# Kernel optimization log

Hardware: AMD Instinct MI355X
Metric: run time of the kernel (lower is better)

The kernel has to match this reference:

```python
import jax, jax.numpy as jnp
import numpy as np

N = 256          # num agents
HID = 128        # hidden_dim
ACT = 5          # action_dim
NH = 4           # num_heads
D = HID + 16     # concat_hidden_dim = 144
E = D * NH       # mha embed dim = 576
HD = D           # per-head dim = E // NH = 144
OBS_RX, OBS_RY = 4, 2   # obs_r from fov_size=(9,5)
GRID = 40


def setup_inputs() -> dict:
    key = jax.random.key(0)
    ks = jax.random.split(key, 24)
    g = lambda k, shape, s: (jax.random.normal(k, shape, dtype=jnp.float32) * s)
    inp = {
        "hidden_state_n": g(ks[0], (N, HID), 1.0),
        "action_n": g(ks[1], (N, HID), 1.0),
        "state_n": jax.random.randint(ks[2], (N, 2), 0, GRID, dtype=jnp.int32),
        # obs encoder
        "W_enc": g(ks[3], (HID, 16), HID ** -0.5), "b_enc": jnp.zeros((16,), jnp.float32),
        # MHABlock outer projections
        "Wq": g(ks[4], (D, E), D ** -0.5), "bq": jnp.zeros((E,), jnp.float32),
        "Wk": g(ks[5], (D, E), D ** -0.5), "bk": jnp.zeros((E,), jnp.float32),
        "Wv": g(ks[6], (D, E), D ** -0.5), "bv": jnp.zeros((E,), jnp.float32),
        # nn.MultiheadAttention internal in/out projections
        "Wiq": g(ks[7], (E, E), E ** -0.5), "biq": jnp.zeros((E,), jnp.float32),
        "Wik": g(ks[8], (E, E), E ** -0.5), "bik": jnp.zeros((E,), jnp.float32),
        "Wiv": g(ks[9], (E, E), E ** -0.5), "biv": jnp.zeros((E,), jnp.float32),
        "Wo_proj": g(ks[10], (E, E), E ** -0.5), "bo_proj": jnp.zeros((E,), jnp.float32),
        "W_O": g(ks[11], (E, D), E ** -0.5),  # no bias
        # dueling decoders
        "W_val": g(ks[12], (D, 1), D ** -0.5), "b_val": jnp.zeros((1,), jnp.float32),
        "W_adv": g(ks[13], (D, ACT), D ** -0.5), "b_adv": jnp.zeros((ACT,), jnp.float32),
    }
    return inp


def reference(hidden_state_n, action_n, W_enc, b_enc, Wq, bq, Wk, bk, Wv, bv,
              Wiq, biq, Wik, bik, Wiv, biv, Wo_proj, bo_proj, W_O,
              W_val, b_val, W_adv, b_adv, state_n):
    n = hidden_state_n.shape[0]
    # observed_agents[i] = {j > i : |x_i-x_j|<=rx and |y_i-y_j|<=ry}
    pos = state_n.astype(jnp.int32)
    dx = jnp.abs(pos[:, None, 0] - pos[None, :, 0])
    dy = jnp.abs(pos[:, None, 1] - pos[None, :, 1])
    upper = jnp.arange(n)[None, :] > jnp.arange(n)[:, None]
    mask = (dx <= OBS_RX) & (dy <= OBS_RY) & upper            # [N,N], mask[i,j]: j observed by i

    # per-neighbor feature c_j = concat(obs_encoder(h_j), a_j)  -> [N, D]
    obs = hidden_state_n @ W_enc + b_enc                       # [N,16]
    C = jnp.concatenate([obs, action_n], axis=-1)              # [N,D]

    # MHABlock: outer Q/K/V projections then nn.MultiheadAttention
    q = (C @ Wq + bq) @ Wiq + biq                              # [N,E]
    k = (C @ Wk + bk) @ Wik + bik
    v = (C @ Wv + bv) @ Wiv + biv
    q2 = q.reshape(n, NH, HD)
    k2 = k.reshape(n, NH, HD)
    v2 = v.reshape(n, NH, HD)

    scale = 1.0 / np.sqrt(HD).astype(np.float32)
    S = jnp.einsum("jhd,khd->hjk", q2, k2) * scale             # [H,N,N] shared across agents

    pair = (mask[:, None, :, None] & mask[:, None, None, :])   # [N,1,Nq,Nk]
    logits = jnp.where(pair, S[None, :, :, :], -1e9)           # [N,H,N,N]
    m = jnp.max(logits, axis=-1, keepdims=True)
    p = jnp.exp(logits - m) * pair.astype(logits.dtype)
    attn = p / jnp.maximum(p.sum(axis=-1, keepdims=True), 1e-9)

    ctx = jnp.einsum("ihjk,khd->ijhd", attn, v2).reshape(n, n, E)  # [N,Nq,E]
    out = (ctx @ Wo_proj + bo_proj) @ W_O                          # [N,Nq,D]

    # sum over the (masked) neighbor/query axis -> per-agent h_i
    h = jnp.sum(out * mask[:, :, None].astype(out.dtype), axis=1)  # [N,D]

    V = h @ W_val + b_val                                          # [N,1]
    A = h @ W_adv + b_adv                                          # [N,ACT]
    Q = V + A - jnp.mean(A, axis=-1, keepdims=True)                # dueling Q
    return Q
```

## Files before the change

### kernel.cpp

```cpp
#include <hip/hip_runtime.h>
#include <hip/hip_bf16.h>

#define NAG 256
#define HID 128
#define ACT 5
#define NH 4
#define DD 144
#define EE 576
#define HDIM 144
#define CMAX 20

template<int KDIM>
__global__ __launch_bounds__(256) void k_gemmK(
    const float* __restrict__ A0, const float* __restrict__ A1, const float* __restrict__ A2,
    const float* __restrict__ W0, const float* __restrict__ W1, const float* __restrict__ W2,
    const float* __restrict__ bb0, const float* __restrict__ bb1, const float* __restrict__ bb2,
    const float* __restrict__ bscale,
    float* __restrict__ o0, float* __restrict__ o1, float* __restrict__ o2,
    int N, int NX)
{
    constexpr int Kc = KDIM / 4;
    constexpr int G  = (Kc % 16 == 0) ? 16 : 12;
    constexpr int NG = Kc / G;
    constexpr int LDA = KDIM + 4;
    __shared__ union { float As[8 * LDA]; float red[2048]; } sm;

    const int perz = NX * 32;
    const int b = blockIdx.x;
    const int z = b / perz, rem = b % perz;
    const int bx = rem >> 5, mb = rem & 31;
    const float* A   = (z == 0) ? A0  : (z == 1) ? A1  : A2;
    const float* W   = (z == 0) ? W0  : (z == 1) ? W1  : W2;
    const float* bia = (z == 0) ? bb0 : (z == 1) ? bb1 : bb2;
    float*       out = (z == 0) ? o0  : (z == 1) ? o1  : o2;
    const int tid = threadIdx.x;

    for (int idx = tid; idx < 8 * (KDIM / 4); idx += 256) {
        int r = idx / (KDIM / 4), c = idx % (KDIM / 4);
        *((float4*)&sm.As[r * LDA + c * 4]) =
            *(const float4*)(A + (size_t)(mb * 8 + r) * KDIM + c * 4);
    }
    __syncthreads();

    const int wave = tid >> 6, lane = tid & 63;
    const int colg = bx * 64 + lane;
    const bool cv = colg < N;
    const int colc = cv ? colg : (N - 1);
    const float* Wp = W + (size_t)(wave * Kc) * N + colc;
    float acc[8] = {};
    float wv[G], wn[G];
    #pragma unroll
    for (int j = 0; j < G; ++j) wv[j] = Wp[(size_t)j * N];
    for (int g = 0; g < NG; ++g) {
        if (g + 1 < NG) {
            const float* Wn = Wp + (size_t)(g + 1) * G * N;
            #pragma unroll
            for (int j = 0; j < G; ++j) wn[j] = Wn[(size_t)j * N];
        }
        const int kb = wave * Kc + g * G;
        #pragma unroll
        for (int j4 = 0; j4 < G / 4; ++j4) {
            #pragma unroll
            for (int r = 0; r < 8; ++r) {
                float4 a4 = *(const float4*)&sm.As[r * LDA + kb + j4 * 4];
                acc[r] += a4.x * wv[j4 * 4 + 0] + a4.y * wv[j4 * 4 + 1]
                        + a4.z * wv[j4 * 4 + 2] + a4.w * wv[j4 * 4 + 3];
            }
        }
        #pragma unroll
        for (int j = 0; j < G; ++j) wv[j] = wn[j];
    }
    __syncthreads();
    #pragma unroll
    for (int r = 0; r < 8; ++r) sm.red[wave * 512 + r * 64 + lane] = acc[r];
    __syncthreads();
    #pragma unroll
    for (int q = 0; q < 2; ++q) {
        int idx = tid + q * 256;
        int r = idx >> 6, cl = idx & 63;
        int col = bx * 64 + cl;
        if (col < N) {
            float s = sm.red[idx] + sm.red[512 + idx]
                    + sm.red[1024 + idx] + sm.red[1536 + idx];
            int row = mb * 8 + r;
            float bs = bscale ? bscale[row] : 1.f;
            float bb = bia ? bia[col] : 0.f;
            out[(size_t)row * N + col] = s + bs * bb;
        }
    }
}

__global__ __launch_bounds__(256) void k_gemm1(
    const float* __restrict__ hidden, const float* __restrict__ action,
    const float* __restrict__ W_enc, const float* __restrict__ b_enc,
    const float* __restrict__ Wq, const float* __restrict__ Wk, const float* __restrict__ Wv,
    const float* __restrict__ bq, const float* __restrict__ bk, const float* __restrict__ bv,
    float* __restrict__ tq, float* __restrict__ tk, float* __restrict__ tv)
{
    __shared__ float Ct[8][148];
    __shared__ union { struct { float Hs[8][132]; float We[2048]; } e;
                       float red[2048]; } u;
    const int b = blockIdx.x;
    const int z = b / 288, rem = b % 288;
    const int bx = rem >> 5, mb = rem & 31;
    const float* W  = (z == 0) ? Wq : (z == 1) ? Wk : Wv;
    const float* bi = (z == 0) ? bq : (z == 1) ? bk : bv;
    float*      out = (z == 0) ? tq : (z == 1) ? tk : tv;
    const int tid = threadIdx.x;

    {
        int r = tid >> 5, kq = tid & 31;
        *((float4*)&u.e.Hs[r][kq * 4]) =
            *(const float4*)(hidden + (mb * 8 + r) * HID + kq * 4);
        *((float4*)&Ct[r][16 + kq * 4]) =
            *(const float4*)(action + (mb * 8 + r) * HID + kq * 4);
        *((float4*)&u.e.We[tid * 4])       = *(const float4*)(W_enc + tid * 4);
        *((float4*)&u.e.We[1024 + tid * 4]) = *(const float4*)(W_enc + 1024 + tid * 4);
    }
    __syncthreads();
    if (tid < 128) {
        int r = tid >> 4, o = tid & 15;
        float acc = 0.f;
        #pragma unroll 8
        for (int d = 0; d < HID; ++d) acc += u.e.Hs[r][d] * u.e.We[d * 16 + o];
        Ct[r][o] = acc + b_enc[o];
    }
    __syncthreads();

    constexpr int Kc = 36, G = 12, NG = 3;
    const int wave = tid >> 6, lane = tid & 63;
    const int colg = bx * 64 + lane;
    const float* Wp = W + (size_t)(wave * Kc) * EE + colg;
    float acc[8] = {};
    float wv[G], wn[G];
    #pragma unroll
    for (int j = 0; j < G; ++j) wv[j] = Wp[(size_t)j * EE];
    for (int g = 0; g < NG; ++g) {
        if (g + 1 < NG) {
            const float* Wn = Wp + (size_t)(g + 1) * G * EE;
            #pragma unroll
            for (int j = 0; j < G; ++j) wn[j] = Wn[(size_t)j * EE];
        }
        const int kb = wave * Kc + g * G;
        #pragma unroll
        for (int j4 = 0; j4 < G / 4; ++j4) {
            #pragma unroll
            for (int r = 0; r < 8; ++r) {
                float4 a4 = *(const float4*)&Ct[r][kb + j4 * 4];
                acc[r] += a4.x * wv[j4 * 4 + 0] + a4.y * wv[j4 * 4 + 1]
                        + a4.z * wv[j4 * 4 + 2] + a4.w * wv[j4 * 4 + 3];
            }
        }
        #pragma unroll
        for (int j = 0; j < G; ++j) wv[j] = wn[j];
    }
    __syncthreads();
    #pragma unroll
    for (int r = 0; r < 8; ++r) u.red[wave * 512 + r * 64 + lane] = acc[r];
    __syncthreads();
    #pragma unroll
    for (int q = 0; q < 2; ++q) {
        int idx = tid + q * 256;
        int r = idx >> 6, cl = idx & 63;
        int col = bx * 64 + cl;
        float s = u.red[idx] + u.red[512 + idx]
                + u.red[1024 + idx] + u.red[1536 + idx];
        out[(size_t)(mb * 8 + r) * EE + col] = s + bi[col];
    }
}

__global__ __launch_bounds__(256) void k_attn(
    const int* __restrict__ state, const float* __restrict__ q,
    const float* __restrict__ kmat, const float* __restrict__ v,
    float* __restrict__ ctxsum, float* __restrict__ cnt)
{
    __shared__ int lst[NAG];
    __shared__ int cnt_s;
    __shared__ float w4[NH][NAG];
    __shared__ float qh[CMAX][HDIM + 1];
    __shared__ float kh[CMAX][HDIM + 1];
    __shared__ float Sl[CMAX][CMAX + 1];
    const int i = blockIdx.x, tid = threadIdx.x;
    if (tid == 0) cnt_s = 0;
    __syncthreads();
    {
        int xi = state[2 * i], yi = state[2 * i + 1];
        int xj = state[2 * tid], yj = state[2 * tid + 1];
        int dx = xi - xj; if (dx < 0) dx = -dx;
        int dy = yi - yj; if (dy < 0) dy = -dy;
        if (tid > i && dx <= 4 && dy <= 2) {
            int p = atomicAdd(&cnt_s, 1);
            lst[p] = tid;
        }
    }
    __syncthreads();
    const int c = cnt_s;
    if (tid == 0) cnt[i] = (float)c;
    if (c == 0) {
        for (int e = tid; e < EE; e += 256) ctxsum[i * EE + e] = 0.f;
        return;
    }
    if (c <= CMAX) {
        for (int h = 0; h < NH; ++h) {
            for (int idx = tid; idx < c * HDIM; idx += 256) {
                int jj = idx / HDIM, d = idx % HDIM;
                qh[jj][d] = q[lst[jj] * EE + h * HDIM + d];
                kh[jj][d] = kmat[lst[jj] * EE + h * HDIM + d];
            }
            __syncthreads();
            for (int pp = tid; pp < c * c; pp += 256) {
                int jj = pp / c, kk = pp % c;
                float acc = 0.f;
                for (int d = 0; d < HDIM; ++d) acc += qh[jj][d] * kh[kk][d];
                Sl[jj][kk] = acc * (1.0f / 12.0f);
            }
            __syncthreads();
            if (tid < c) {
                float m = -1e30f;
                for (int kk = 0; kk < c; ++kk) m = fmaxf(m, Sl[tid][kk]);
                float zz = 0.f;
                for (int kk = 0; kk < c; ++kk) zz += __expf(Sl[tid][kk] - m);
                float inv = 1.f / fmaxf(zz, 1e-9f);
                for (int kk = 0; kk < c; ++kk)
                    Sl[tid][kk] = __expf(Sl[tid][kk] - m) * inv;
            }
            __syncthreads();
            if (tid < c) {
                float s = 0.f;
                for (int jj = 0; jj < c; ++jj) s += Sl[jj][tid];
                w4[h][tid] = s;
            }
            __syncthreads();
        }
    } else {
        for (int idx = tid; idx < NH * c; idx += 256) w4[idx / c][idx % c] = 0.f;
        __syncthreads();
        for (int pnh = tid; pnh < NH * c; pnh += 256) {
            int h = pnh / c, jj = pnh % c;
            const float* qrow = q + lst[jj] * EE + h * HDIM;
            float m = -1e30f;
            for (int kk = 0; kk < c; ++kk) {
                const float* krow = kmat + lst[kk] * EE + h * HDIM;
                float a = 0.f;
                for (int d = 0; d < HDIM; ++d) a += qrow[d] * krow[d];
                m = fmaxf(m, a * (1.0f / 12.0f));
            }
            float zz = 0.f;
            for (int kk = 0; kk < c; ++kk) {
                const float* krow = kmat + lst[kk] * EE + h * HDIM;
                float a = 0.f;
                for (int d = 0; d < HDIM; ++d) a += qrow[d] * krow[d];
                zz += __expf(a * (1.0f / 12.0f) - m);
            }
            float inv = 1.f / fmaxf(zz, 1e-9f);
            for (int kk = 0; kk < c; ++kk) {
                const float* krow = kmat + lst[kk] * EE + h * HDIM;
                float a = 0.f;
                for (int d = 0; d < HDIM; ++d) a += qrow[d] * krow[d];
                atomicAdd(&w4[h][kk], __expf(a * (1.0f / 12.0f) - m) * inv);
            }
        }
        __syncthreads();
    }
    for (int e = tid; e < EE; e += 256) {
        int h = e / HDIM;
        float acc = 0.f;
        for (int t = 0; t < c; ++t) acc += w4[h][t] * v[lst[t] * EE + e];
        ctxsum[i * EE + e] = acc;
    }
}

__global__ __launch_bounds__(64) void k_head(
    const float* __restrict__ hb,
    const float* __restrict__ W_val, const float* __restrict__ b_val,
    const float* __restrict__ W_adv, const float* __restrict__ b_adv,
    float* __restrict__ out)
{
    const int i = blockIdx.x, t = threadIdx.x;
    const float* hr = hb + i * DD;
    float h0 = hr[t], h1 = hr[t + 64];
    float h2 = (t < 16) ? hr[t + 128] : 0.f;
    float red[6];
    for (int o = 0; o < 6; ++o) {
        float p;
        if (o < 5) {
            p = h0 * W_adv[t * ACT + o] + h1 * W_adv[(t + 64) * ACT + o];
            if (t < 16) p += h2 * W_adv[(t + 128) * ACT + o];
        } else {
            p = h0 * W_val[t] + h1 * W_val[t + 64];
            if (t < 16) p += h2 * W_val[t + 128];
        }
        for (int off = 32; off; off >>= 1) p += __shfl_xor(p, off);
        red[o] = p;
    }
    if (t == 0) {
        float a[ACT], mean = 0.f;
        for (int o = 0; o < ACT; ++o) { a[o] = red[o] + b_adv[o]; mean += a[o]; }
        mean *= (1.0f / ACT);
        float V = red[5] + b_val[0];
        for (int o = 0; o < ACT; ++o) out[i * ACT + o] = V + a[o] - mean;
    }
}

extern "C" void kernel_launch(void* const* d_in, const int* in_sizes, int n_in,
                              void* d_out, int out_size, void* d_ws, size_t ws_size,
                              hipStream_t stream)
{
    const float* hidden = (const float*)d_in[0];
    const float* action = (const float*)d_in[1];
    const int*   state  = (const int*)d_in[2];

    float* ws = (float*)d_ws;
    float* tq   = ws;
    float* tk   = tq   + NAG * EE;
    float* tv   = tk   + NAG * EE;
    float* q    = tv   + NAG * EE;
    float* kb   = q    + NAG * EE;
    float* v    = kb   + NAG * EE;
    float* ctx  = v    + NAG * EE;
    float* cnt  = ctx  + NAG * EE;
    float* hbuf = cnt  + NAG;
    float* tout = tq;

    k_gemm1<<<864, 256, 0, stream>>>(hidden, action,
        (const float*)d_in[3], (const float*)d_in[4],
        (const float*)d_in[5], (const float*)d_in[7], (const float*)d_in[9],
        (const float*)d_in[6], (const float*)d_in[8], (const float*)d_in[10],
        tq, tk, tv);

    k_gemmK<576><<<864, 256, 0, stream>>>(tq, tk, tv,
        (const float*)d_in[11], (const float*)d_in[13], (const float*)d_in[15],
        (const float*)d_in[12], (const float*)d_in[14], (const float*)d_in[16],
        nullptr, q, kb, v, EE, 9);

    k_attn<<<NAG, 256, 0, stream>>>(state, q, kb, v, ctx, cnt);

    k_gemmK<576><<<288, 256, 0, stream>>>(ctx, ctx, ctx,
        (const float*)d_in[17], (const float*)d_in[17], (const float*)d_in[17],
        (const float*)d_in[18], (const float*)d_in[18], (const float*)d_in[18],
        cnt, tout, tout, tout, EE, 9);

    k_gemmK<576><<<96, 256, 0, stream>>>(tout, tout, tout,
        (const float*)d_in[19], (const float*)d_in[19], (const float*)d_in[19],
        nullptr, nullptr, nullptr,
        nullptr, hbuf, hbuf, hbuf, DD, 3);

    k_head<<<NAG, 64, 0, stream>>>(hbuf,
        (const float*)d_in[20], (const float*)d_in[21],
        (const float*)d_in[22], (const float*)d_in[23], (float*)d_out);
}
```

Baseline: 192.1 us.

## Prefetch later-stage weights into L2 via extra blocks and enlarge register weight groups

Extra blocks are appended to the first GEMM and the attention kernel. They read the weights used by the next stage (Wiq/Wik/Wiv, then Wo_proj/W_O) so those matrices sit in cache when the following kernels run, with a dummy conditional store to keep the loads alive. The GEMM inner loops now load all 36 weight rows per wave into registers at once instead of double-buffering groups of 12 or 16. The context accumulation loop is split across two accumulators to expose more memory-level parallelism. The extra blocks add launch work and memory traffic, and the larger register arrays may lower occupancy.

```diff
diff --git a/kernel.cpp b/kernel.cpp
--- a/kernel.cpp
+++ b/kernel.cpp
@@ -20,7 +20,7 @@
     int N, int NX)
 {
     constexpr int Kc = KDIM / 4;
-    constexpr int G  = (Kc % 16 == 0) ? 16 : 12;
+    constexpr int G  = 36;
     constexpr int NG = Kc / G;
     constexpr int LDA = KDIM + 4;
     __shared__ union { float As[8 * LDA]; float red[2048]; } sm;
@@ -95,18 +95,34 @@
     const float* __restrict__ W_enc, const float* __restrict__ b_enc,
     const float* __restrict__ Wq, const float* __restrict__ Wk, const float* __restrict__ Wv,
     const float* __restrict__ bq, const float* __restrict__ bk, const float* __restrict__ bv,
-    float* __restrict__ tq, float* __restrict__ tk, float* __restrict__ tv)
-{
+    const float* __restrict__ Wiq, const float* __restrict__ Wik, const float* __restrict__ Wiv,
+    float* __restrict__ tq, float* __restrict__ tk, float* __restrict__ tv,
+    float* __restrict__ sink)
+{
+    const int b = blockIdx.x;
+    const int tid = threadIdx.x;
+    if (b >= 864) {
+        const int wb = b - 864;
+        float s = 0.f;
+        for (int m = 0; m < 3; ++m) {
+            const float* Wm = (m == 0) ? Wiq : (m == 1) ? Wik : Wiv;
+            const float4* W4 = (const float4*)Wm;
+            for (int idx = wb * 324 + tid; idx < (wb + 1) * 324 && idx < 82944; idx += 256) {
+                float4 v4 = W4[idx];
+                s += v4.x + v4.y + v4.z + v4.w;
+            }
+        }
+        if (s == 123456789.0f) sink[0] = s;
+        return;
+    }
     __shared__ float Ct[8][148];
     __shared__ union { struct { float Hs[8][132]; float We[2048]; } e;
                        float red[2048]; } u;
-    const int b = blockIdx.x;
     const int z = b / 288, rem = b % 288;
     const int bx = rem >> 5, mb = rem & 31;
     const float* W  = (z == 0) ? Wq : (z == 1) ? Wk : Wv;
     const float* bi = (z == 0) ? bq : (z == 1) ? bk : bv;
     float*      out = (z == 0) ? tq : (z == 1) ? tk : tv;
-    const int tid = threadIdx.x;
 
     {
         int r = tid >> 5, kq = tid & 31;
@@ -114,7 +130,7 @@
             *(const float4*)(hidden + (mb * 8 + r) * HID + kq * 4);
         *((float4*)&Ct[r][16 + kq * 4]) =
             *(const float4*)(action + (mb * 8 + r) * HID + kq * 4);
-        *((float4*)&u.e.We[tid * 4])       = *(const float4*)(W_enc + tid * 4);
+        *((float4*)&u.e.We[tid * 4])        = *(const float4*)(W_enc + tid * 4);
         *((float4*)&u.e.We[1024 + tid * 4]) = *(const float4*)(W_enc + 1024 + tid * 4);
     }
     __syncthreads();
@@ -127,32 +143,23 @@
     }
     __syncthreads();
 
-    constexpr int Kc = 36, G = 12, NG = 3;
+    constexpr int Kc = 36, G = 36;
     const int wave = tid >> 6, lane = tid & 63;
     const int colg = bx * 64 + lane;
     const float* Wp = W + (size_t)(wave * Kc) * EE + colg;
     float acc[8] = {};
-    float wv[G], wn[G];
+    float wv[G];
     #pragma unroll
     for (int j = 0; j < G; ++j) wv[j] = Wp[(size_t)j * EE];
-    for (int g = 0; g < NG; ++g) {
-        if (g + 1 < NG) {
-            const float* Wn = Wp + (size_t)(g + 1) * G * EE;
-            #pragma unroll
-            for (int j = 0; j < G; ++j) wn[j] = Wn[(size_t)j * EE];
-        }
-        const int kb = wave * Kc + g * G;
+    const int kb = wave * Kc;
+    #pragma unroll
+    for (int j4 = 0; j4 < G / 4; ++j4) {
         #pragma unroll
-        for (int j4 = 0; j4 < G / 4; ++j4) {
-            #pragma unroll
-            for (int r = 0; r < 8; ++r) {
-                float4 a4 = *(const float4*)&Ct[r][kb + j4 * 4];
-                acc[r] += a4.x * wv[j4 * 4 + 0] + a4.y * wv[j4 * 4 + 1]
-                        + a4.z * wv[j4 * 4 + 2] + a4.w * wv[j4 * 4 + 3];
-            }
-        }
-        #pragma unroll
-        for (int j = 0; j < G; ++j) wv[j] = wn[j];
+        for (int r = 0; r < 8; ++r) {
+            float4 a4 = *(const float4*)&Ct[r][kb + j4 * 4];
+            acc[r] += a4.x * wv[j4 * 4 + 0] + a4.y * wv[j4 * 4 + 1]
+                    + a4.z * wv[j4 * 4 + 2] + a4.w * wv[j4 * 4 + 3];
+        }
     }
     __syncthreads();
     #pragma unroll
@@ -172,15 +179,34 @@
 __global__ __launch_bounds__(256) void k_attn(
     const int* __restrict__ state, const float* __restrict__ q,
     const float* __restrict__ kmat, const float* __restrict__ v,
-    float* __restrict__ ctxsum, float* __restrict__ cnt)
-{
+    const float* __restrict__ Wo, const float* __restrict__ W_O,
+    float* __restrict__ ctxsum, float* __restrict__ cnt,
+    float* __restrict__ sink)
+{
+    const int blk = blockIdx.x, tid = threadIdx.x;
+    if (blk >= NAG) {
+        const int wb = blk - NAG;
+        float s = 0.f;
+        const float4* W4 = (const float4*)Wo;
+        for (int idx = wb * 324 + tid; idx < (wb + 1) * 324 && idx < 82944; idx += 256) {
+            float4 v4 = W4[idx];
+            s += v4.x + v4.y + v4.z + v4.w;
+        }
+        const float4* O4 = (const float4*)W_O;
+        for (int idx = wb * 81 + tid; idx < (wb + 1) * 81 && idx < 20736; idx += 256) {
+            float4 v4 = O4[idx];
+            s += v4.x + v4.y + v4.z + v4.w;
+        }
+        if (s == 123456789.0f) sink[1] = s;
+        return;
+    }
     __shared__ int lst[NAG];
     __shared__ int cnt_s;
     __shared__ float w4[NH][NAG];
     __shared__ float qh[CMAX][HDIM + 1];
     __shared__ float kh[CMAX][HDIM + 1];
     __shared__ float Sl[CMAX][CMAX + 1];
-    const int i = blockIdx.x, tid = threadIdx.x;
+    const int i = blk;
     if (tid == 0) cnt_s = 0;
     __syncthreads();
     {
@@ -264,9 +290,14 @@
     }
     for (int e = tid; e < EE; e += 256) {
         int h = e / HDIM;
-        float acc = 0.f;
-        for (int t = 0; t < c; ++t) acc += w4[h][t] * v[lst[t] * EE + e];
-        ctxsum[i * EE + e] = acc;
+        float a0 = 0.f, a1 = 0.f;
+        int t = 0;
+        for (; t + 1 < c; t += 2) {
+            a0 += w4[h][t] * v[lst[t] * EE + e];
+            a1 += w4[h][t + 1] * v[lst[t + 1] * EE + e];
+        }
+        if (t < c) a0 += w4[h][t] * v[lst[t] * EE + e];
+        ctxsum[i * EE + e] = a0 + a1;
     }
 }
 
@@ -320,20 +351,23 @@
     float* ctx  = v    + NAG * EE;
     float* cnt  = ctx  + NAG * EE;
     float* hbuf = cnt  + NAG;
+    float* sink = hbuf + NAG * DD;
     float* tout = tq;
 
-    k_gemm1<<<864, 256, 0, stream>>>(hidden, action,
+    k_gemm1<<<1120, 256, 0, stream>>>(hidden, action,
         (const float*)d_in[3], (const float*)d_in[4],
         (const float*)d_in[5], (const float*)d_in[7], (const float*)d_in[9],
         (const float*)d_in[6], (const float*)d_in[8], (const float*)d_in[10],
-        tq, tk, tv);
+        (const float*)d_in[11], (const float*)d_in[13], (const float*)d_in[15],
+        tq, tk, tv, sink);
 
     k_gemmK<576><<<864, 256, 0, stream>>>(tq, tk, tv,
         (const float*)d_in[11], (const float*)d_in[13], (const float*)d_in[15],
         (const float*)d_in[12], (const float*)d_in[14], (const float*)d_in[16],
         nullptr, q, kb, v, EE, 9);
 
-    k_attn<<<NAG, 256, 0, stream>>>(state, q, kb, v, ctx, cnt);
+    k_attn<<<512, 256, 0, stream>>>(state, q, kb, v,
+        (const float*)d_in[17], (const float*)d_in[19], ctx, cnt, sink);
 
     k_gemmK<576><<<288, 256, 0, stream>>>(ctx, ctx, ctx,
         (const float*)d_in[17], (const float*)d_in[17], (const float*)d_in[17],
```

Result: no change. 192.8 us (+0.3%).

## Remap GEMM blocks across XCDs and load whole weight slices at once

Applied to the files above, without the earlier changes.

Block indices are remapped so the 8 row-blocks sharing the same weight column tile run on the same XCD (p&7 picks the column group). This is meant to improve L2 reuse of weights, at the cost of padded grids where some blocks exit early. The weight register group grows to 36, so each wave loads its whole K-slice in one batch instead of double-buffered groups, which raises register pressure. The attention context accumulation is also split into two independent accumulators to add ILP.

```diff
diff --git a/kernel.cpp b/kernel.cpp
--- a/kernel.cpp
+++ b/kernel.cpp
@@ -10,25 +10,27 @@
 #define HDIM 144
 #define CMAX 20
 
-template<int KDIM>
+template<int KDIM, int AG, int NX, int GSLOTS>
 __global__ __launch_bounds__(256) void k_gemmK(
     const float* __restrict__ A0, const float* __restrict__ A1, const float* __restrict__ A2,
     const float* __restrict__ W0, const float* __restrict__ W1, const float* __restrict__ W2,
     const float* __restrict__ bb0, const float* __restrict__ bb1, const float* __restrict__ bb2,
     const float* __restrict__ bscale,
     float* __restrict__ o0, float* __restrict__ o1, float* __restrict__ o2,
-    int N, int NX)
+    int N)
 {
     constexpr int Kc = KDIM / 4;
-    constexpr int G  = (Kc % 16 == 0) ? 16 : 12;
+    constexpr int G  = 36;
     constexpr int NG = Kc / G;
     constexpr int LDA = KDIM + 4;
     __shared__ union { float As[8 * LDA]; float red[2048]; } sm;
 
-    const int perz = NX * 32;
-    const int b = blockIdx.x;
-    const int z = b / perz, rem = b % perz;
-    const int bx = rem >> 5, mb = rem & 31;
+    const int p = blockIdx.x;
+    const int xcd = p & 7, qq = p >> 3;
+    const int mb = qq & 31, gslot = qq >> 5;
+    const int g = xcd + 8 * gslot;
+    if (g >= AG) return;
+    const int bx = g % NX, z = g / NX;
     const float* A   = (z == 0) ? A0  : (z == 1) ? A1  : A2;
     const float* W   = (z == 0) ? W0  : (z == 1) ? W1  : W2;
     const float* bia = (z == 0) ? bb0 : (z == 1) ? bb1 : bb2;
@@ -51,13 +53,13 @@
     float wv[G], wn[G];
     #pragma unroll
     for (int j = 0; j < G; ++j) wv[j] = Wp[(size_t)j * N];
-    for (int g = 0; g < NG; ++g) {
-        if (g + 1 < NG) {
-            const float* Wn = Wp + (size_t)(g + 1) * G * N;
+    for (int gi = 0; gi < NG; ++gi) {
+        if (gi + 1 < NG) {
+            const float* Wn = Wp + (size_t)(gi + 1) * G * N;
             #pragma unroll
             for (int j = 0; j < G; ++j) wn[j] = Wn[(size_t)j * N];
         }
-        const int kb = wave * Kc + g * G;
+        const int kb = wave * Kc + gi * G;
         #pragma unroll
         for (int j4 = 0; j4 < G / 4; ++j4) {
             #pragma unroll
@@ -97,24 +99,27 @@
     const float* __restrict__ bq, const float* __restrict__ bk, const float* __restrict__ bv,
     float* __restrict__ tq, float* __restrict__ tk, float* __restrict__ tv)
 {
-    __shared__ float Ct[8][148];
-    __shared__ union { struct { float Hs[8][132]; float We[2048]; } e;
-                       float red[2048]; } u;
-    const int b = blockIdx.x;
-    const int z = b / 288, rem = b % 288;
-    const int bx = rem >> 5, mb = rem & 31;
+    const int p = blockIdx.x;
+    const int xcd = p & 7, qq = p >> 3;
+    const int mb = qq & 31, gslot = qq >> 5;
+    const int g = xcd + 8 * gslot;
+    if (g >= 27) return;
+    const int bx = g % 9, z = g / 9;
     const float* W  = (z == 0) ? Wq : (z == 1) ? Wk : Wv;
     const float* bi = (z == 0) ? bq : (z == 1) ? bk : bv;
     float*      out = (z == 0) ? tq : (z == 1) ? tk : tv;
     const int tid = threadIdx.x;
 
+    __shared__ float Ct[8][148];
+    __shared__ union { struct { float Hs[8][132]; float We[2048]; } e;
+                       float red[2048]; } u;
     {
         int r = tid >> 5, kq = tid & 31;
         *((float4*)&u.e.Hs[r][kq * 4]) =
             *(const float4*)(hidden + (mb * 8 + r) * HID + kq * 4);
         *((float4*)&Ct[r][16 + kq * 4]) =
             *(const float4*)(action + (mb * 8 + r) * HID + kq * 4);
-        *((float4*)&u.e.We[tid * 4])       = *(const float4*)(W_enc + tid * 4);
+        *((float4*)&u.e.We[tid * 4])        = *(const float4*)(W_enc + tid * 4);
         *((float4*)&u.e.We[1024 + tid * 4]) = *(const float4*)(W_enc + 1024 + tid * 4);
     }
     __syncthreads();
@@ -127,32 +132,23 @@
     }
     __syncthreads();
 
-    constexpr int Kc = 36, G = 12, NG = 3;
+    constexpr int Kc = 36, G = 36;
     const int wave = tid >> 6, lane = tid & 63;
     const int colg = bx * 64 + lane;
     const float* Wp = W + (size_t)(wave * Kc) * EE + colg;
     float acc[8] = {};
-    float wv[G], wn[G];
+    float wv[G];
     #pragma unroll
     for (int j = 0; j < G; ++j) wv[j] = Wp[(size_t)j * EE];
-    for (int g = 0; g < NG; ++g) {
-        if (g + 1 < NG) {
-            const float* Wn = Wp + (size_t)(g + 1) * G * EE;
-            #pragma unroll
-            for (int j = 0; j < G; ++j) wn[j] = Wn[(size_t)j * EE];
-        }
-        const int kb = wave * Kc + g * G;
+    const int kb = wave * Kc;
+    #pragma unroll
+    for (int j4 = 0; j4 < G / 4; ++j4) {
         #pragma unroll
-        for (int j4 = 0; j4 < G / 4; ++j4) {
-            #pragma unroll
-            for (int r = 0; r < 8; ++r) {
-                float4 a4 = *(const float4*)&Ct[r][kb + j4 * 4];
-                acc[r] += a4.x * wv[j4 * 4 + 0] + a4.y * wv[j4 * 4 + 1]
-                        + a4.z * wv[j4 * 4 + 2] + a4.w * wv[j4 * 4 + 3];
-            }
-        }
-        #pragma unroll
-        for (int j = 0; j < G; ++j) wv[j] = wn[j];
+        for (int r = 0; r < 8; ++r) {
+            float4 a4 = *(const float4*)&Ct[r][kb + j4 * 4];
+            acc[r] += a4.x * wv[j4 * 4 + 0] + a4.y * wv[j4 * 4 + 1]
+                    + a4.z * wv[j4 * 4 + 2] + a4.w * wv[j4 * 4 + 3];
+        }
     }
     __syncthreads();
     #pragma unroll
@@ -264,9 +260,14 @@
     }
     for (int e = tid; e < EE; e += 256) {
         int h = e / HDIM;
-        float acc = 0.f;
-        for (int t = 0; t < c; ++t) acc += w4[h][t] * v[lst[t] * EE + e];
-        ctxsum[i * EE + e] = acc;
+        float a0 = 0.f, a1 = 0.f;
+        int t = 0;
+        for (; t + 1 < c; t += 2) {
+            a0 += w4[h][t] * v[lst[t] * EE + e];
+            a1 += w4[h][t + 1] * v[lst[t + 1] * EE + e];
+        }
+        if (t < c) a0 += w4[h][t] * v[lst[t] * EE + e];
+        ctxsum[i * EE + e] = a0 + a1;
     }
 }
 
@@ -322,28 +323,28 @@
     float* hbuf = cnt  + NAG;
     float* tout = tq;
 
-    k_gemm1<<<864, 256, 0, stream>>>(hidden, action,
+    k_gemm1<<<1024, 256, 0, stream>>>(hidden, action,
         (const float*)d_in[3], (const float*)d_in[4],
         (const float*)d_in[5], (const float*)d_in[7], (const float*)d_in[9],
         (const float*)d_in[6], (const float*)d_in[8], (const float*)d_in[10],
         tq, tk, tv);
 
-    k_gemmK<576><<<864, 256, 0, stream>>>(tq, tk, tv,
+    k_gemmK<576, 27, 9, 4><<<1024, 256, 0, stream>>>(tq, tk, tv,
         (const float*)d_in[11], (const float*)d_in[13], (const float*)d_in[15],
         (const float*)d_in[12], (const float*)d_in[14], (const float*)d_in[16],
-        nullptr, q, kb, v, EE, 9);
+        nullptr, q, kb, v, EE);
 
     k_attn<<<NAG, 256, 0, stream>>>(state, q, kb, v, ctx, cnt);
 
-    k_gemmK<576><<<288, 256, 0, stream>>>(ctx, ctx, ctx,
+    k_gemmK<576, 9, 9, 2><<<512, 256, 0, stream>>>(ctx, ctx, ctx,
         (const float*)d_in[17], (const float*)d_in[17], (const float*)d_in[17],
         (const float*)d_in[18], (const float*)d_in[18], (const float*)d_in[18],
-        cnt, tout, tout, tout, EE, 9);
-
-    k_gemmK<576><<<96, 256, 0, stream>>>(tout, tout, tout,
+        cnt, tout, tout, tout, EE);
+
+    k_gemmK<576, 3, 3, 1><<<256, 256, 0, stream>>>(tout, tout, tout,
         (const float*)d_in[19], (const float*)d_in[19], (const float*)d_in[19],
         nullptr, nullptr, nullptr,
-        nullptr, hbuf, hbuf, hbuf, DD, 3);
+        nullptr, hbuf, hbuf, hbuf, DD);
 
     k_head<<<NAG, 64, 0, stream>>>(hbuf,
         (const float*)d_in[20], (const float*)d_in[21],
```

After: 194.7 us. Within noise of the previous version (+1.3%).
